# Kernel optimization log

Measured on AMD Instinct MI355X. Metric: run time of the kernel, lower is better.

Reference implementation:

```python
import jax, jax.numpy as jnp
import numpy as np

H = 512   # hidden_size
E = 256   # embedding_size
V = 32000 # vocab_size
L = 1024  # max_length (encoder seq len)
B = 64    # batch


def setup_inputs() -> dict:
    key = jax.random.key(0)
    ks = jax.random.split(key, 18)
    n = lambda i, shape, s=0.05: (jax.random.normal(ks[i], shape, dtype=jnp.float32) * s)
    return {
        "input": jax.random.randint(ks[0], (B, 1), 0, V),
        "last_output_context": n(1, (1, B, H), 1.0),
        "last_hidden": n(2, (1, B, H), 1.0),
        "last_cell_state": n(3, (1, B, H), 1.0),
        "encoder_outputs": n(4, (L, B, H), 1.0),
        "emb": n(5, (V, E)),
        "W_ih": n(6, (4 * H, E + H)),
        "W_hh": n(7, (4 * H, H)),
        "b_ih": n(8, (4 * H,)),
        "b_hh": n(9, (4 * H,)),
        "W_attn": n(10, (H, 2 * H)),
        "b_attn": n(11, (H,)),
        "beta": n(12, (H, 1), 1.0),
        "W_oc": n(13, (H, 2 * H)),
        "b_oc": n(14, (H,)),
        "W_out": n(15, (V, H)),
        "b_out": n(16, (V,)),
    }


def reference(input, last_output_context, last_hidden, last_cell_state,
              encoder_outputs, emb, W_ih, W_hh, b_ih, b_hh,
              W_attn, b_attn, beta, W_oc, b_oc, W_out, b_out):
    # embedding lookup: (B,1) -> (B,E)  (permute(1,0,2) then squeeze step dim)
    tok = emb[input[:, 0]]                                   # (B, E)
    x = jnp.concatenate([tok, last_output_context[0]], axis=1)  # (B, E+H)
    # single-step LSTM (PyTorch gate order i, f, g, o)
    gates = x @ W_ih.T + last_hidden[0] @ W_hh.T + b_ih + b_hh  # (B, 4H)
    i_g, f_g, g_g, o_g = jnp.split(gates, 4, axis=1)
    i_g = jax.nn.sigmoid(i_g)
    f_g = jax.nn.sigmoid(f_g)
    g_g = jnp.tanh(g_g)
    o_g = jax.nn.sigmoid(o_g)
    c = f_g * last_cell_state[0] + i_g * g_g                  # (B, H)
    h = o_g * jnp.tanh(c)                                     # (B, H) == rnn_output
    # additive attention, vectorized over the seq_len loop
    h_tiled = jnp.broadcast_to(h[None], (L, B, H))
    cat = jnp.concatenate([h_tiled, encoder_outputs], axis=-1)  # (L, B, 2H)
    energy = jnp.tanh(cat @ W_attn.T + b_attn) @ beta           # (L, B, 1)
    attn_w = jax.nn.softmax(energy[..., 0], axis=0)             # (L, B) softmax over seq
    # context = bmm(attn_weights, encoder_outputs)
    context = jnp.einsum('lb,lbh->bh', attn_w, encoder_outputs)  # (B, H)
    co = jnp.tanh(jnp.concatenate([h, context], axis=1) @ W_oc.T + b_oc)  # (B, H)
    output = jax.nn.log_softmax(co @ W_out.T + b_out, axis=1)    # (B, V)
    return output, co[None], h[None], c[None]
```

## Files before the change

### kernel.cpp

```cpp
#include <hip/hip_runtime.h>
#include <hip/hip_bf16.h>
#include <cstddef>

#define H   512
#define E   256
#define V   32000
#define L   1024
#define B   64
#define KX  768
#define M_TOT 65536

typedef __attribute__((ext_vector_type(8))) _Float16 half8v;
typedef __attribute__((ext_vector_type(4))) float f32x4;

__device__ __forceinline__ half8v cvt8(float4 x0, float4 x1) {
    union { half8v v; _Float16 u[8]; } hv;
    hv.u[0] = (_Float16)x0.x; hv.u[1] = (_Float16)x0.y;
    hv.u[2] = (_Float16)x0.z; hv.u[3] = (_Float16)x0.w;
    hv.u[4] = (_Float16)x1.x; hv.u[5] = (_Float16)x1.y;
    hv.u[6] = (_Float16)x1.z; hv.u[7] = (_Float16)x1.w;
    return hv.v;
}

__device__ __forceinline__ void glds16(const void* g, void* l) {
    __builtin_amdgcn_global_load_lds(
        (const __attribute__((address_space(1))) void*)g,
        (__attribute__((address_space(3))) void*)l, 16, 0, 0);
}

__global__ __launch_bounds__(256) void k_prep(const float* __restrict__ W_attn,
                                              unsigned short* __restrict__ WfB,
                                              const int* __restrict__ inp,
                                              const float* __restrict__ loc,
                                              const float* __restrict__ hprev,
                                              const float* __restrict__ emb,
                                              float* __restrict__ xprevT) {
    if (blockIdx.x < 128) {
        int u = blockIdx.x * 256 + threadIdx.x;
        int lane = u & 63;
        int rest = u >> 6;
        int f = rest & 7;
        int kt = (rest >> 3) & 15;
        int jt = rest >> 7;
        int wn = f >> 2, nf = f & 3;
        int j = jt * 128 + wn * 64 + nf * 16 + (lane & 15);
        int col = kt * 32 + (lane >> 4) * 8;
        const float* src = &W_attn[(size_t)j * (2 * H) + H + col];
        float4 x0 = *reinterpret_cast<const float4*>(src);
        float4 x1 = *reinterpret_cast<const float4*>(src + 4);
        *reinterpret_cast<half8v*>(&WfB[(size_t)u * 8]) = cvt8(x0, x1);
    } else {
        int gid = (blockIdx.x - 128) * 256 + threadIdx.x;
        int k = gid >> 6, b = gid & 63;
        float v;
        if (k < 256)      v = emb[(size_t)inp[b] * E + k];
        else if (k < 768) v = loc[b * H + (k - 256)];
        else              v = hprev[b * H + (k - 768)];
        xprevT[gid] = v;
    }
}

__global__ __launch_bounds__(256) void k_lstm(const float* __restrict__ W_ih,
                                              const float* __restrict__ W_hh,
                                              const float* __restrict__ b_ih,
                                              const float* __restrict__ b_hh,
                                              const float* __restrict__ xprevT,
                                              const float* __restrict__ cprev,
                                              float* __restrict__ h_out,
                                              float* __restrict__ c_out,
                                              float* __restrict__ hnewT) {
    int u = blockIdx.x;
    int w = threadIdx.x >> 6;
    int b = threadIdx.x & 63;
    int j = w * 512 + u;
    float a0 = 0.f, a1 = 0.f, a2 = 0.f, a3 = 0.f;
    const float* Wr = &W_ih[(size_t)j * KX];
    for (int k = 0; k < KX; k += 4) {
        float4 wv = *reinterpret_cast<const float4*>(&Wr[k]);
        a0 += wv.x * xprevT[(k + 0) * 64 + b];
        a1 += wv.y * xprevT[(k + 1) * 64 + b];
        a2 += wv.z * xprevT[(k + 2) * 64 + b];
        a3 += wv.w * xprevT[(k + 3) * 64 + b];
    }
    const float* Wr2 = &W_hh[(size_t)j * H];
    const float* hT = &xprevT[KX * 64];
    for (int k = 0; k < H; k += 4) {
        float4 wv = *reinterpret_cast<const float4*>(&Wr2[k]);
        a0 += wv.x * hT[(k + 0) * 64 + b];
        a1 += wv.y * hT[(k + 1) * 64 + b];
        a2 += wv.z * hT[(k + 2) * 64 + b];
        a3 += wv.w * hT[(k + 3) * 64 + b];
    }
    float acc = b_ih[j] + b_hh[j] + ((a0 + a1) + (a2 + a3));
    __shared__ float gs[4][64];
    gs[w][b] = acc;
    __syncthreads();
    if (threadIdx.x < 64) {
        float ig = 1.f / (1.f + __expf(-gs[0][b]));
        float fg = 1.f / (1.f + __expf(-gs[1][b]));
        float gg = tanhf(gs[2][b]);
        float og = 1.f / (1.f + __expf(-gs[3][b]));
        float c = fg * cprev[b * H + u] + ig * gg;
        float h = og * tanhf(c);
        c_out[b * H + u] = c;
        h_out[b * H + u] = h;
        hnewT[u * 64 + b] = h;
    }
}

__global__ __launch_bounds__(256) void k_hw(const float* __restrict__ W_attn,
                                            const float* __restrict__ b_attn,
                                            const float* __restrict__ hT,
                                            float* __restrict__ hW_jb) {
    int j = blockIdx.x * 4 + (threadIdx.x >> 6);
    int b = threadIdx.x & 63;
    float a0 = 0.f, a1 = 0.f, a2 = 0.f, a3 = 0.f;
    const float* Wr = &W_attn[(size_t)j * (2 * H)];
    for (int k = 0; k < H; k += 4) {
        float4 wv = *reinterpret_cast<const float4*>(&Wr[k]);
        a0 += wv.x * hT[(k + 0) * 64 + b];
        a1 += wv.y * hT[(k + 1) * 64 + b];
        a2 += wv.z * hT[(k + 2) * 64 + b];
        a3 += wv.w * hT[(k + 3) * 64 + b];
    }
    hW_jb[j * 64 + b] = b_attn[j] + ((a0 + a1) + (a2 + a3));
}

__global__ __launch_bounds__(256, 4) void k_energy_v12(
        const float* __restrict__ enc,
        const unsigned short* __restrict__ WfB,
        const float* __restrict__ hW,
        const float* __restrict__ beta,
        float* __restrict__ partial_e) {
    __shared__ float Af[4096];
    __shared__ unsigned short Bh2[4096];
    __shared__ float red[2][128];

    const int tid  = threadIdx.x;
    const int lane = tid & 63;
    const int w    = tid >> 6;
    const int wm = w >> 1;
    const int wn = w & 1;
    const int bid = blockIdx.x;
    const int xcd = bid & 7;
    const int loc = bid >> 3;
    const int mt  = xcd * 64 + (loc >> 2);
    const int jt  = loc & 3;
    const int m0 = mt * 128;
    const int j0 = jt * 128;

    const int fr = lane & 15;
    const int g  = lane >> 4;

    const float* asrcA[4];
    #pragma unroll
    for (int i = 0; i < 4; ++i) {
        int c0 = (w * 4 + i) * 64 + lane;
        int row = c0 >> 3;
        int sc = (lane & 7) ^ (row & 7);
        asrcA[i] = enc + (size_t)(m0 + row) * H + sc * 4;
    }
    const size_t bbase = (size_t)jt * 16 * 512;

    f32x4 acc[4][4];
    #pragma unroll
    for (int i = 0; i < 4; ++i)
        #pragma unroll
        for (int j = 0; j < 4; ++j) acc[i][j] = (f32x4){0.f, 0.f, 0.f, 0.f};

    for (int kt = 0; kt < 16; ++kt) {
        #pragma unroll
        for (int i = 0; i < 4; ++i)
            glds16(asrcA[i] + kt * 32, &Af[((w * 4 + i) * 64 + lane) * 4]);
        #pragma unroll
        for (int i = 0; i < 2; ++i)
            glds16(WfB + (bbase + (size_t)kt * 512 + (w * 2 + i) * 64 + lane) * 8,
                   &Bh2[((w * 2 + i) * 64 + lane) * 8]);
        __syncthreads();
        half8v a_h[4], b_h[4];
        #pragma unroll
        for (int mf = 0; mf < 4; ++mf) {
            int R = wm * 64 + mf * 16 + fr;
            int p0 = (2 * g) ^ (R & 7);
            int p1 = p0 ^ 1;
            float4 f0 = *reinterpret_cast<const float4*>(&Af[(R * 8 + p0) * 4]);
            float4 f1 = *reinterpret_cast<const float4*>(&Af[(R * 8 + p1) * 4]);
            a_h[mf] = cvt8(f0, f1);
        }
        #pragma unroll
        for (int nf = 0; nf < 4; ++nf)
            b_h[nf] = *reinterpret_cast<const half8v*>(
                &Bh2[((wn * 4 + nf) * 64 + lane) * 8]);
        #pragma unroll
        for (int mf = 0; mf < 4; ++mf)
            #pragma unroll
            for (int nf = 0; nf < 4; ++nf)
                acc[mf][nf] = __builtin_amdgcn_mfma_f32_16x16x32_f16(
                    a_h[mf], b_h[nf], acc[mf][nf], 0, 0, 0);
        __syncthreads();
    }

    float psum[4][4];
    #pragma unroll
    for (int i = 0; i < 4; ++i)
        #pragma unroll
        for (int r = 0; r < 4; ++r) psum[i][r] = 0.f;
    #pragma unroll
    for (int nf = 0; nf < 4; ++nf) {
        int jj = j0 + wn * 64 + nf * 16 + (lane & 15);
        float bet = beta[jj];
        #pragma unroll
        for (int mf = 0; mf < 4; ++mf) {
            int b_base = (wm * 64 + mf * 16 + (lane >> 4) * 4) & 63;
            float4 hw4 = *reinterpret_cast<const float4*>(&hW[jj * 64 + b_base]);
            float hwv[4] = {hw4.x, hw4.y, hw4.z, hw4.w};
            #pragma unroll
            for (int r = 0; r < 4; ++r) {
                float e = acc[mf][nf][r] + hwv[r];
                float ex = __expf(2.f * e);
                psum[mf][r] += bet * (1.f - 2.f / (ex + 1.f));
            }
        }
    }
    #pragma unroll
    for (int mf = 0; mf < 4; ++mf)
        #pragma unroll
        for (int r = 0; r < 4; ++r) {
            float v = psum[mf][r];
            v += __shfl_xor(v, 1);
            v += __shfl_xor(v, 2);
            v += __shfl_xor(v, 4);
            v += __shfl_xor(v, 8);
            psum[mf][r] = v;
        }
    __syncthreads();
    if ((lane & 15) == 0) {
        #pragma unroll
        for (int mf = 0; mf < 4; ++mf)
            #pragma unroll
            for (int r = 0; r < 4; ++r)
                red[wn][wm * 64 + mf * 16 + (lane >> 4) * 4 + r] = psum[mf][r];
    }
    __syncthreads();
    if (tid < 128)
        partial_e[(size_t)jt * M_TOT + m0 + tid] = red[0][tid] + red[1][tid];
}

__global__ __launch_bounds__(256) void k_softmax_l(const float* __restrict__ partial_e,
                                                   float* __restrict__ attn_w) {
    int b = blockIdx.x;
    int tid = threadIdx.x;
    float el[4];
    float m = -1e30f;
    #pragma unroll
    for (int i = 0; i < 4; ++i) {
        int l = i * 256 + tid;
        float e = 0.f;
        #pragma unroll
        for (int nb = 0; nb < 4; ++nb)
            e += partial_e[(size_t)nb * M_TOT + l * 64 + b];
        el[i] = e;
        m = fmaxf(m, e);
    }
    #pragma unroll
    for (int s = 1; s < 64; s <<= 1) m = fmaxf(m, __shfl_xor(m, s));
    __shared__ float redm[4];
    if ((tid & 63) == 0) redm[tid >> 6] = m;
    __syncthreads();
    m = fmaxf(fmaxf(redm[0], redm[1]), fmaxf(redm[2], redm[3]));
    float s = 0.f;
    #pragma unroll
    for (int i = 0; i < 4; ++i) { el[i] = __expf(el[i] - m); s += el[i]; }
    #pragma unroll
    for (int sh = 1; sh < 64; sh <<= 1) s += __shfl_xor(s, sh);
    __shared__ float reds[4];
    if ((tid & 63) == 0) reds[tid >> 6] = s;
    __syncthreads();
    s = reds[0] + reds[1] + reds[2] + reds[3];
    float inv = 1.f / s;
    #pragma unroll
    for (int i = 0; i < 4; ++i)
        attn_w[(i * 256 + tid) * 64 + b] = el[i] * inv;
}

__global__ __launch_bounds__(128) void k_ctx_part(const float* __restrict__ attn_w,
                                                  const float* __restrict__ enc,
                                                  float* __restrict__ ctx_part) {
    int chunk = blockIdx.x, b = blockIdx.y;
    int h = threadIdx.x * 4;
    float4 acc = {0.f, 0.f, 0.f, 0.f};
    for (int i = 0; i < 32; ++i) {
        int l = chunk * 32 + i;
        float w = attn_w[l * 64 + b];
        float4 e4 = *reinterpret_cast<const float4*>(
            &enc[((size_t)l * 64 + b) * H + h]);
        acc.x += w * e4.x;
        acc.y += w * e4.y;
        acc.z += w * e4.z;
        acc.w += w * e4.w;
    }
    *reinterpret_cast<float4*>(&ctx_part[((size_t)(chunk * 64 + b)) * H + h]) = acc;
}

__global__ __launch_bounds__(256) void k_ctx_reduce(const float* __restrict__ ctx_part,
                                                    float* __restrict__ ctxT) {
    int gid = blockIdx.x * 256 + threadIdx.x;
    int b = gid >> 9, h = gid & 511;
    float s = 0.f;
    for (int c = 0; c < 32; ++c)
        s += ctx_part[((size_t)(c * 64 + b)) * H + h];
    ctxT[h * 64 + b] = s;
}

__global__ __launch_bounds__(256) void k_co(const float* __restrict__ W_oc,
                                            const float* __restrict__ b_oc,
                                            const float* __restrict__ hT,
                                            const float* __restrict__ ctxT,
                                            float* __restrict__ co_out) {
    int j = blockIdx.x * 4 + (threadIdx.x >> 6);
    int b = threadIdx.x & 63;
    float a0 = 0.f, a1 = 0.f, a2 = 0.f, a3 = 0.f;
    const float* Wr = &W_oc[(size_t)j * (2 * H)];
    for (int k = 0; k < H; k += 4) {
        float4 wv = *reinterpret_cast<const float4*>(&Wr[k]);
        a0 += wv.x * hT[(k + 0) * 64 + b];
        a1 += wv.y * hT[(k + 1) * 64 + b];
        a2 += wv.z * hT[(k + 2) * 64 + b];
        a3 += wv.w * hT[(k + 3) * 64 + b];
    }
    const float* Wr2 = Wr + H;
    for (int k = 0; k < H; k += 4) {
        float4 wv = *reinterpret_cast<const float4*>(&Wr2[k]);
        a0 += wv.x * ctxT[(k + 0) * 64 + b];
        a1 += wv.y * ctxT[(k + 1) * 64 + b];
        a2 += wv.z * ctxT[(k + 2) * 64 + b];
        a3 += wv.w * ctxT[(k + 3) * 64 + b];
    }
    co_out[b * H + j] = tanhf(b_oc[j] + ((a0 + a1) + (a2 + a3)));
}

__global__ __launch_bounds__(256) void k_logits_v3(const float* __restrict__ co,
                                                   const float* __restrict__ W_out,
                                                   const float* __restrict__ b_out,
                                                   float* __restrict__ logits) {
    const int tid  = threadIdx.x;
    const int lane = tid & 63;
    const int w    = tid >> 6;
    const int fr   = lane & 15;
    const int kb   = (lane >> 4) * 8;
    const int j    = blockIdx.x * 64 + w * 16 + fr;

    f32x4 acc[4];
    #pragma unroll
    for (int mf = 0; mf < 4; ++mf) acc[mf] = (f32x4){0.f, 0.f, 0.f, 0.f};

    const float* Arow = &co[(size_t)fr * H + kb];
    const float* Brow = &W_out[(size_t)j * H + kb];

    for (int k0 = 0; k0 < H; k0 += 32) {
        float4 b0 = *reinterpret_cast<const float4*>(Brow + k0);
        float4 b1 = *reinterpret_cast<const float4*>(Brow + k0 + 4);
        half8v bh = cvt8(b0, b1);
        #pragma unroll
        for (int mf = 0; mf < 4; ++mf) {
            const float* ap = Arow + (size_t)mf * 16 * H + k0;
            float4 a0 = *reinterpret_cast<const float4*>(ap);
            float4 a1 = *reinterpret_cast<const float4*>(ap + 4);
            half8v ah = cvt8(a0, a1);
            acc[mf] = __builtin_amdgcn_mfma_f32_16x16x32_f16(ah, bh, acc[mf], 0, 0, 0);
        }
    }
    float bo = b_out[j];
    #pragma unroll
    for (int mf = 0; mf < 4; ++mf) {
        int mbase = mf * 16 + (lane >> 4) * 4;
        #pragma unroll
        for (int r = 0; r < 4; ++r)
            logits[(size_t)(mbase + r) * V + j] = acc[mf][r] + bo;
    }
}

__global__ __launch_bounds__(256) void k_lsm_part(const float* __restrict__ logits,
                                                  float* __restrict__ pmax,
                                                  float* __restrict__ psum) {
    int chunk = blockIdx.x, b = blockIdx.y;
    int tid = threadIdx.x;
    const float* row = &logits[(size_t)b * V + chunk * 4000];
    float v[16];
    float m = -1e30f;
    #pragma unroll
    for (int t = 0; t < 16; ++t) {
        int i = t * 256 + tid;
        v[t] = (i < 4000) ? row[i] : -1e30f;
        m = fmaxf(m, v[t]);
    }
    #pragma unroll
    for (int s = 1; s < 64; s <<= 1) m = fmaxf(m, __shfl_xor(m, s));
    __shared__ float redm[4];
    if ((tid & 63) == 0) redm[tid >> 6] = m;
    __syncthreads();
    m = fmaxf(fmaxf(redm[0], redm[1]), fmaxf(redm[2], redm[3]));
    float s = 0.f;
    #pragma unroll
    for (int t = 0; t < 16; ++t) s += __expf(v[t] - m);
    #pragma unroll
    for (int sh = 1; sh < 64; sh <<= 1) s += __shfl_xor(s, sh);
    __shared__ float reds[4];
    if ((tid & 63) == 0) reds[tid >> 6] = s;
    __syncthreads();
    if (tid == 0) {
        pmax[chunk * 64 + b] = m;
        psum[chunk * 64 + b] = reds[0] + reds[1] + reds[2] + reds[3];
    }
}

__global__ __launch_bounds__(256) void k_lsm_write(const float* __restrict__ logits,
                                                   const float* __restrict__ pmax,
                                                   const float* __restrict__ psum,
                                                   float* __restrict__ out) {
    size_t i4 = ((size_t)blockIdx.x * 256 + threadIdx.x) * 4;
    int b = (int)(i4 / V);
    float m = -1e30f;
    #pragma unroll
    for (int c = 0; c < 8; ++c) m = fmaxf(m, pmax[c * 64 + b]);
    float s = 0.f;
    #pragma unroll
    for (int c = 0; c < 8; ++c) s += psum[c * 64 + b] * __expf(pmax[c * 64 + b] - m);
    float l = m + __logf(s);
    float4 x = *reinterpret_cast<const float4*>(&logits[i4]);
    x.x -= l; x.y -= l; x.z -= l; x.w -= l;
    *reinterpret_cast<float4*>(&out[i4]) = x;
}

extern "C" void kernel_launch(void* const* d_in, const int* in_sizes, int n_in,
                              void* d_out, int out_size, void* d_ws, size_t ws_size,
                              hipStream_t stream) {
    const int*   inp    = (const int*)  d_in[0];
    const float* loc    = (const float*)d_in[1];
    const float* hprev  = (const float*)d_in[2];
    const float* cprev  = (const float*)d_in[3];
    const float* enc    = (const float*)d_in[4];
    const float* emb    = (const float*)d_in[5];
    const float* W_ih   = (const float*)d_in[6];
    const float* W_hh   = (const float*)d_in[7];
    const float* b_ih   = (const float*)d_in[8];
    const float* b_hh   = (const float*)d_in[9];
    const float* W_attn = (const float*)d_in[10];
    const float* b_attn = (const float*)d_in[11];
    const float* beta   = (const float*)d_in[12];
    const float* W_oc   = (const float*)d_in[13];
    const float* b_oc   = (const float*)d_in[14];
    const float* W_out  = (const float*)d_in[15];
    const float* b_out  = (const float*)d_in[16];

    float* out = (float*)d_out;
    float* out_co = out + (size_t)B * V;
    float* out_h  = out_co + B * H;
    float* out_c  = out_h  + B * H;

    float* ws = (float*)d_ws;
    float* xprevT = ws;
    float* hnewT  = xprevT + 1280 * 64;
    float* hW     = hnewT  + H * 64;
    float* pe     = hW     + H * 64;
    float* attnw  = pe     + 4 * M_TOT;
    float* ctxp   = attnw  + M_TOT;
    float* ctxT   = ctxp   + 32 * 64 * H;
    float* logits = ctxT   + H * 64;
    float* pmax   = logits + (size_t)B * V;
    float* psum   = pmax   + 512;
    float* lse    = psum   + 512;
    unsigned short* WfB = (unsigned short*)(lse + 64);

    k_prep  <<<448, 256, 0, stream>>>(W_attn, WfB, inp, loc, hprev, emb, xprevT);
    k_lstm  <<<512, 256, 0, stream>>>(W_ih, W_hh, b_ih, b_hh, xprevT, cprev,
                                      out_h, out_c, hnewT);
    k_hw    <<<128, 256, 0, stream>>>(W_attn, b_attn, hnewT, hW);
    k_energy_v12<<<2048, 256, 0, stream>>>(enc, WfB, hW, beta, pe);
    k_softmax_l<<<64, 256, 0, stream>>>(pe, attnw);
    k_ctx_part <<<dim3(32, 64), 128, 0, stream>>>(attnw, enc, ctxp);
    k_ctx_reduce<<<128, 256, 0, stream>>>(ctxp, ctxT);
    k_co    <<<128, 256, 0, stream>>>(W_oc, b_oc, hnewT, ctxT, out_co);
    k_logits_v3<<<500, 256, 0, stream>>>(out_co, W_out, b_out, logits);
    k_lsm_part<<<dim3(8, 64), 256, 0, stream>>>(logits, pmax, psum);
    k_lsm_write<<<2000, 256, 0, stream>>>(logits, pmax, psum, out);
}
```

Before: 254.3 us.

## Double-buffer LDS tiles in attention energy GEMM to overlap loads with MFMA

The energy kernel now keeps two LDS buffers for the encoder and weight tiles and issues the global-to-LDS copy for the next k-step before computing on the current one. This is meant to hide global memory latency behind the MFMA work. The cost is doubled LDS use per block and a lower occupancy hint (3 blocks per CU instead of 4), and the k loop is fully unrolled.

```diff
diff --git a/kernel.cpp b/kernel.cpp
--- a/kernel.cpp
+++ b/kernel.cpp
@@ -126,14 +126,14 @@
     hW_jb[j * 64 + b] = b_attn[j] + ((a0 + a1) + (a2 + a3));
 }
 
-__global__ __launch_bounds__(256, 4) void k_energy_v12(
+__global__ __launch_bounds__(256, 3) void k_energy_v13(
         const float* __restrict__ enc,
         const unsigned short* __restrict__ WfB,
         const float* __restrict__ hW,
         const float* __restrict__ beta,
         float* __restrict__ partial_e) {
-    __shared__ float Af[4096];
-    __shared__ unsigned short Bh2[4096];
+    __shared__ float Af[2][4096];
+    __shared__ unsigned short Bh2[2][4096];
     __shared__ float red[2][128];
 
     const int tid  = threadIdx.x;
@@ -162,35 +162,46 @@
     }
     const size_t bbase = (size_t)jt * 16 * 512;
 
+#define STAGE(buf, kt)                                                          \
+    {                                                                           \
+        _Pragma("unroll")                                                       \
+        for (int i = 0; i < 4; ++i)                                             \
+            glds16(asrcA[i] + (kt) * 32,                                        \
+                   &Af[buf][((w * 4 + i) * 64 + lane) * 4]);                    \
+        _Pragma("unroll")                                                       \
+        for (int i = 0; i < 2; ++i)                                             \
+            glds16(WfB + (bbase + (size_t)(kt) * 512 + (w * 2 + i) * 64 + lane) * 8, \
+                   &Bh2[buf][((w * 2 + i) * 64 + lane) * 8]);                   \
+    }
+
     f32x4 acc[4][4];
     #pragma unroll
     for (int i = 0; i < 4; ++i)
         #pragma unroll
         for (int j = 0; j < 4; ++j) acc[i][j] = (f32x4){0.f, 0.f, 0.f, 0.f};
 
+    STAGE(0, 0)
+    __syncthreads();
+
+    #pragma unroll
     for (int kt = 0; kt < 16; ++kt) {
-        #pragma unroll
-        for (int i = 0; i < 4; ++i)
-            glds16(asrcA[i] + kt * 32, &Af[((w * 4 + i) * 64 + lane) * 4]);
-        #pragma unroll
-        for (int i = 0; i < 2; ++i)
-            glds16(WfB + (bbase + (size_t)kt * 512 + (w * 2 + i) * 64 + lane) * 8,
-                   &Bh2[((w * 2 + i) * 64 + lane) * 8]);
-        __syncthreads();
+        const int cur = kt & 1;
+        const int nxt = cur ^ 1;
+        if (kt + 1 < 16) STAGE(nxt, kt + 1)
         half8v a_h[4], b_h[4];
         #pragma unroll
         for (int mf = 0; mf < 4; ++mf) {
             int R = wm * 64 + mf * 16 + fr;
             int p0 = (2 * g) ^ (R & 7);
             int p1 = p0 ^ 1;
-            float4 f0 = *reinterpret_cast<const float4*>(&Af[(R * 8 + p0) * 4]);
-            float4 f1 = *reinterpret_cast<const float4*>(&Af[(R * 8 + p1) * 4]);
+            float4 f0 = *reinterpret_cast<const float4*>(&Af[cur][(R * 8 + p0) * 4]);
+            float4 f1 = *reinterpret_cast<const float4*>(&Af[cur][(R * 8 + p1) * 4]);
             a_h[mf] = cvt8(f0, f1);
         }
         #pragma unroll
         for (int nf = 0; nf < 4; ++nf)
             b_h[nf] = *reinterpret_cast<const half8v*>(
-                &Bh2[((wn * 4 + nf) * 64 + lane) * 8]);
+                &Bh2[cur][((wn * 4 + nf) * 64 + lane) * 8]);
         #pragma unroll
         for (int mf = 0; mf < 4; ++mf)
             #pragma unroll
@@ -476,7 +487,7 @@
     k_lstm  <<<512, 256, 0, stream>>>(W_ih, W_hh, b_ih, b_hh, xprevT, cprev,
                                       out_h, out_c, hnewT);
     k_hw    <<<128, 256, 0, stream>>>(W_attn, b_attn, hnewT, hW);
-    k_energy_v12<<<2048, 256, 0, stream>>>(enc, WfB, hW, beta, pe);
+    k_energy_v13<<<2048, 256, 0, stream>>>(enc, WfB, hW, beta, pe);
     k_softmax_l<<<64, 256, 0, stream>>>(pe, attnw);
     k_ctx_part <<<dim3(32, 64), 128, 0, stream>>>(attnw, enc, ctxp);
     k_ctx_reduce<<<128, 256, 0, stream>>>(ctxp, ctxT);
```

Measured after the change: 260.5 us. +2.4%, slower.

## Compute LSTM gates with fp16 MFMA and split epilogue kernel

Applied to the files above, without the earlier changes.

Replaces the scalar FP32 LSTM gate GEMV kernel with an MFMA-based kernel that converts weights and a new row-major copy of the inputs to fp16. Gates go to a workspace buffer, and a separate elementwise kernel applies the activations and the cell update. The energy kernel's launch bound also rises from 4 to 6 waves per SIMD to raise occupancy. The fp16 conversion lowers gate precision, and only 32 blocks read the 6 MB of weights, so bandwidth use may be limited.

```diff
diff --git a/kernel.cpp b/kernel.cpp
--- a/kernel.cpp
+++ b/kernel.cpp
@@ -8,6 +8,7 @@
 #define L   1024
 #define B   64
 #define KX  768
+#define G2  2048
 #define M_TOT 65536
 
 typedef __attribute__((ext_vector_type(8))) _Float16 half8v;
@@ -34,7 +35,8 @@
                                               const float* __restrict__ loc,
                                               const float* __restrict__ hprev,
                                               const float* __restrict__ emb,
-                                              float* __restrict__ xprevT) {
+                                              float* __restrict__ xprevT,
+                                              float* __restrict__ xprev_rm) {
     if (blockIdx.x < 128) {
         int u = blockIdx.x * 256 + threadIdx.x;
         int lane = u & 63;
@@ -57,55 +59,83 @@
         else if (k < 768) v = loc[b * H + (k - 256)];
         else              v = hprev[b * H + (k - 768)];
         xprevT[gid] = v;
-    }
-}
-
-__global__ __launch_bounds__(256) void k_lstm(const float* __restrict__ W_ih,
-                                              const float* __restrict__ W_hh,
-                                              const float* __restrict__ b_ih,
-                                              const float* __restrict__ b_hh,
-                                              const float* __restrict__ xprevT,
-                                              const float* __restrict__ cprev,
-                                              float* __restrict__ h_out,
-                                              float* __restrict__ c_out,
-                                              float* __restrict__ hnewT) {
-    int u = blockIdx.x;
-    int w = threadIdx.x >> 6;
-    int b = threadIdx.x & 63;
-    int j = w * 512 + u;
-    float a0 = 0.f, a1 = 0.f, a2 = 0.f, a3 = 0.f;
-    const float* Wr = &W_ih[(size_t)j * KX];
-    for (int k = 0; k < KX; k += 4) {
-        float4 wv = *reinterpret_cast<const float4*>(&Wr[k]);
-        a0 += wv.x * xprevT[(k + 0) * 64 + b];
-        a1 += wv.y * xprevT[(k + 1) * 64 + b];
-        a2 += wv.z * xprevT[(k + 2) * 64 + b];
-        a3 += wv.w * xprevT[(k + 3) * 64 + b];
-    }
-    const float* Wr2 = &W_hh[(size_t)j * H];
-    const float* hT = &xprevT[KX * 64];
-    for (int k = 0; k < H; k += 4) {
-        float4 wv = *reinterpret_cast<const float4*>(&Wr2[k]);
-        a0 += wv.x * hT[(k + 0) * 64 + b];
-        a1 += wv.y * hT[(k + 1) * 64 + b];
-        a2 += wv.z * hT[(k + 2) * 64 + b];
-        a3 += wv.w * hT[(k + 3) * 64 + b];
-    }
-    float acc = b_ih[j] + b_hh[j] + ((a0 + a1) + (a2 + a3));
-    __shared__ float gs[4][64];
-    gs[w][b] = acc;
-    __syncthreads();
-    if (threadIdx.x < 64) {
-        float ig = 1.f / (1.f + __expf(-gs[0][b]));
-        float fg = 1.f / (1.f + __expf(-gs[1][b]));
-        float gg = tanhf(gs[2][b]);
-        float og = 1.f / (1.f + __expf(-gs[3][b]));
-        float c = fg * cprev[b * H + u] + ig * gg;
-        float h = og * tanhf(c);
-        c_out[b * H + u] = c;
-        h_out[b * H + u] = h;
-        hnewT[u * 64 + b] = h;
-    }
+        xprev_rm[b * 1280 + k] = v;
+    }
+}
+
+__global__ __launch_bounds__(256) void k_lstm_mfma(const float* __restrict__ xprev_rm,
+                                                   const float* __restrict__ W_ih,
+                                                   const float* __restrict__ W_hh,
+                                                   const float* __restrict__ b_ih,
+                                                   const float* __restrict__ b_hh,
+                                                   float* __restrict__ gates) {
+    const int tid  = threadIdx.x;
+    const int lane = tid & 63;
+    const int w    = tid >> 6;
+    const int fr   = lane & 15;
+    const int kb   = (lane >> 4) * 8;
+    const int j    = blockIdx.x * 64 + w * 16 + fr;
+
+    f32x4 acc[4];
+    #pragma unroll
+    for (int mf = 0; mf < 4; ++mf) acc[mf] = (f32x4){0.f, 0.f, 0.f, 0.f};
+
+    const float* Arow = xprev_rm + (size_t)fr * 1280 + kb;
+    const float* Brow1 = W_ih + (size_t)j * KX + kb;
+    for (int k0 = 0; k0 < KX; k0 += 32) {
+        float4 b0 = *reinterpret_cast<const float4*>(Brow1 + k0);
+        float4 b1 = *reinterpret_cast<const float4*>(Brow1 + k0 + 4);
+        half8v bh = cvt8(b0, b1);
+        #pragma unroll
+        for (int mf = 0; mf < 4; ++mf) {
+            const float* ap = Arow + (size_t)mf * 16 * 1280 + k0;
+            float4 a0 = *reinterpret_cast<const float4*>(ap);
+            float4 a1 = *reinterpret_cast<const float4*>(ap + 4);
+            acc[mf] = __builtin_amdgcn_mfma_f32_16x16x32_f16(
+                cvt8(a0, a1), bh, acc[mf], 0, 0, 0);
+        }
+    }
+    const float* Brow2 = W_hh + (size_t)j * H + kb;
+    for (int k0 = 0; k0 < H; k0 += 32) {
+        float4 b0 = *reinterpret_cast<const float4*>(Brow2 + k0);
+        float4 b1 = *reinterpret_cast<const float4*>(Brow2 + k0 + 4);
+        half8v bh = cvt8(b0, b1);
+        #pragma unroll
+        for (int mf = 0; mf < 4; ++mf) {
+            const float* ap = Arow + (size_t)mf * 16 * 1280 + KX + k0;
+            float4 a0 = *reinterpret_cast<const float4*>(ap);
+            float4 a1 = *reinterpret_cast<const float4*>(ap + 4);
+            acc[mf] = __builtin_amdgcn_mfma_f32_16x16x32_f16(
+                cvt8(a0, a1), bh, acc[mf], 0, 0, 0);
+        }
+    }
+    float bo = b_ih[j] + b_hh[j];
+    #pragma unroll
+    for (int mf = 0; mf < 4; ++mf) {
+        int mbase = mf * 16 + (lane >> 4) * 4;
+        #pragma unroll
+        for (int r = 0; r < 4; ++r)
+            gates[(size_t)(mbase + r) * G2 + j] = acc[mf][r] + bo;
+    }
+}
+
+__global__ __launch_bounds__(256) void k_lstm_ep(const float* __restrict__ gates,
+                                                 const float* __restrict__ cprev,
+                                                 float* __restrict__ h_out,
+                                                 float* __restrict__ c_out,
+                                                 float* __restrict__ hnewT) {
+    int gid = blockIdx.x * 256 + threadIdx.x;
+    int b = gid >> 9, u = gid & 511;
+    const float* gr = &gates[(size_t)b * G2];
+    float ig = 1.f / (1.f + __expf(-gr[u]));
+    float fg = 1.f / (1.f + __expf(-gr[u + 512]));
+    float gg = tanhf(gr[u + 1024]);
+    float og = 1.f / (1.f + __expf(-gr[u + 1536]));
+    float c = fg * cprev[b * H + u] + ig * gg;
+    float h = og * tanhf(c);
+    c_out[b * H + u] = c;
+    h_out[b * H + u] = h;
+    hnewT[u * 64 + b] = h;
 }
 
 __global__ __launch_bounds__(256) void k_hw(const float* __restrict__ W_attn,
@@ -126,7 +156,7 @@
     hW_jb[j * 64 + b] = b_attn[j] + ((a0 + a1) + (a2 + a3));
 }
 
-__global__ __launch_bounds__(256, 4) void k_energy_v12(
+__global__ __launch_bounds__(256, 6) void k_energy_v14(
         const float* __restrict__ enc,
         const unsigned short* __restrict__ WfB,
         const float* __restrict__ hW,
@@ -459,24 +489,26 @@
     float* out_c  = out_h  + B * H;
 
     float* ws = (float*)d_ws;
-    float* xprevT = ws;
-    float* hnewT  = xprevT + 1280 * 64;
-    float* hW     = hnewT  + H * 64;
-    float* pe     = hW     + H * 64;
-    float* attnw  = pe     + 4 * M_TOT;
-    float* ctxp   = attnw  + M_TOT;
-    float* ctxT   = ctxp   + 32 * 64 * H;
-    float* logits = ctxT   + H * 64;
-    float* pmax   = logits + (size_t)B * V;
-    float* psum   = pmax   + 512;
-    float* lse    = psum   + 512;
-    unsigned short* WfB = (unsigned short*)(lse + 64);
-
-    k_prep  <<<448, 256, 0, stream>>>(W_attn, WfB, inp, loc, hprev, emb, xprevT);
-    k_lstm  <<<512, 256, 0, stream>>>(W_ih, W_hh, b_ih, b_hh, xprevT, cprev,
-                                      out_h, out_c, hnewT);
+    float* xprevT  = ws;
+    float* xprev_rm = xprevT + 1280 * 64;
+    float* hnewT   = xprev_rm + 1280 * 64;
+    float* hW      = hnewT  + H * 64;
+    float* gates   = hW     + H * 64;
+    float* pe      = gates  + B * G2;
+    float* attnw   = pe     + 4 * M_TOT;
+    float* ctxp    = attnw  + M_TOT;
+    float* ctxT    = ctxp   + 32 * 64 * H;
+    float* logits  = ctxT   + H * 64;
+    float* pmax    = logits + (size_t)B * V;
+    float* psum    = pmax   + 512;
+    unsigned short* WfB = (unsigned short*)(psum + 512);
+
+    k_prep  <<<448, 256, 0, stream>>>(W_attn, WfB, inp, loc, hprev, emb,
+                                      xprevT, xprev_rm);
+    k_lstm_mfma<<<32, 256, 0, stream>>>(xprev_rm, W_ih, W_hh, b_ih, b_hh, gates);
+    k_lstm_ep<<<128, 256, 0, stream>>>(gates, cprev, out_h, out_c, hnewT);
     k_hw    <<<128, 256, 0, stream>>>(W_attn, b_attn, hnewT, hW);
-    k_energy_v12<<<2048, 256, 0, stream>>>(enc, WfB, hW, beta, pe);
+    k_energy_v14<<<2048, 256, 0, stream>>>(enc, WfB, hW, beta, pe);
     k_softmax_l<<<64, 256, 0, stream>>>(pe, attnw);
     k_ctx_part <<<dim3(32, 64), 128, 0, stream>>>(attnw, enc, ctxp);
     k_ctx_reduce<<<128, 256, 0, stream>>>(ctxp, ctxT);
```

Result: slower. 521.1 us (+104.9%).
